# Kernel tuning notes

Measured on AMD Instinct MI355X. Metric: run time of the kernel, lower is better.

## Reference

```python
import jax, jax.numpy as jnp
import numpy as np

B, K, F_DIM, H_DIM, HEADS = 512, 17, 256, 256, 4
N = B * K           # 8704 flattened nodes
E = 139264          # edges (avg degree 16)
NEG_SLOPE = 0.2


def setup_inputs() -> dict:
    key = jax.random.key(0)
    ks = jax.random.split(key, 12)
    s_in = 1.0 / np.sqrt(F_DIM)
    s_hid = 1.0 / np.sqrt(H_DIM)
    return {
        "kpt_feature": jax.random.normal(ks[0], (B, K, F_DIM), jnp.float32),
        "edge_index": jax.random.randint(ks[1], (2, E), 0, N, jnp.int64),
        # conv1: F_DIM -> HEADS x H_DIM, concat=False (mean)
        "W1": jax.random.normal(ks[2], (F_DIM, HEADS * H_DIM), jnp.float32) * s_in,
        "a_src1": jax.random.normal(ks[3], (HEADS, H_DIM), jnp.float32) * s_hid,
        "a_dst1": jax.random.normal(ks[4], (HEADS, H_DIM), jnp.float32) * s_hid,
        "b1": jnp.zeros((H_DIM,), jnp.float32),
        # conv2: H_DIM -> HEADS x F_DIM, concat=False (mean)
        "W2": jax.random.normal(ks[5], (H_DIM, HEADS * F_DIM), jnp.float32) * s_hid,
        "a_src2": jax.random.normal(ks[6], (HEADS, F_DIM), jnp.float32) * s_in,
        "a_dst2": jax.random.normal(ks[7], (HEADS, F_DIM), jnp.float32) * s_in,
        "b2": jnp.zeros((F_DIM,), jnp.float32),
    }


def gat_conv(x, src, dst, W, a_src, a_dst, bias):
    # x: [N, Fin]; src/dst: [E'] (self-loops included); W: [Fin, H*C]
    n = x.shape[0]
    heads, c = a_src.shape
    h = (x @ W).reshape(n, heads, c)                       # [N,H,C]
    alpha_src = jnp.einsum("nhc,hc->nh", h, a_src)         # [N,H]
    alpha_dst = jnp.einsum("nhc,hc->nh", h, a_dst)
    e = jax.nn.leaky_relu(alpha_src[src] + alpha_dst[dst], NEG_SLOPE)  # [E',H]
    # segment softmax over incoming edges of each destination node
    emax = jax.ops.segment_max(e, dst, num_segments=n)
    emax = jnp.where(jnp.isfinite(emax), emax, 0.0)
    ex = jnp.exp(e - emax[dst])
    denom = jax.ops.segment_sum(ex, dst, num_segments=n)
    alpha = ex / denom[dst]                                # [E',H]
    msg = alpha[:, :, None] * h[src]                       # [E',H,C]
    out = jax.ops.segment_sum(msg, dst, num_segments=n)    # [N,H,C]
    return out.mean(axis=1) + bias                         # concat=False -> mean


def reference(kpt_feature, edge_index, W1, a_src1, a_dst1, b1, W2, a_src2, a_dst2, b2):
    b, k, f = kpt_feature.shape
    n = b * k
    x = kpt_feature.reshape(n, f)
    loop = jnp.arange(n, dtype=edge_index.dtype)
    src = jnp.concatenate([edge_index[0], loop])  # PyG add_self_loops=True
    dst = jnp.concatenate([edge_index[1], loop])
    x = gat_conv(x, src, dst, W1, a_src1, a_dst1, b1)
    x = jax.nn.relu(x)
    x = gat_conv(x, src, dst, W2, a_src2, a_dst2, b2)
    return x.reshape(b, k, f)
```

## Files before the change

kernel.cpp:

```cpp
#include <hip/hip_runtime.h>
#include <hip/hip_fp16.h>
#include <math.h>

#define NNODES 8704
#define NEDGE  139264
#define EPLUS  (NEDGE + NNODES)
#define NEG_SLOPE 0.2f
#define DEGCAP 64
#define LDSK   40

#define NB_PV  16
#define NB_WC  512
#define NB_SC  ((EPLUS + 255) / 256)
#define NB_AL  (NNODES / 4)

typedef _Float16 f16x8 __attribute__((ext_vector_type(8)));
typedef _Float16 f16x4 __attribute__((ext_vector_type(4)));
typedef float    f32x4 __attribute__((ext_vector_type(4)));

__device__ __forceinline__ float lrelu(float v) { return v >= 0.f ? v : NEG_SLOPE * v; }

__global__ __launch_bounds__(256) void prep_all(const float* __restrict__ W1,
                                                const float* __restrict__ as1,
                                                const float* __restrict__ ad1,
                                                const float* __restrict__ W2,
                                                const float* __restrict__ as2,
                                                const float* __restrict__ ad2,
                                                float* __restrict__ pbuf,
                                                int* __restrict__ cnt,
                                                float* __restrict__ alphasB,
                                                _Float16* __restrict__ Wc1,
                                                _Float16* __restrict__ Wc2) {
    __shared__ float tile[32][33];
    const int b = blockIdx.x;
    const int t = threadIdx.x;
    if (b < NB_PV) {
        for (int i = b * 256 + t; i < NNODES; i += NB_PV * 256) cnt[i] = 0;
        for (int i = b * 256 + t; i < NNODES * 8; i += NB_PV * 256) alphasB[i] = 0.f;
        float* a_sh = &tile[0][0];
        const int layer = b >> 3, sd = (b >> 2) & 1, h = b & 3;
        const float* W  = layer ? W2 : W1;
        const float* av = layer ? (sd ? ad2 : as2) : (sd ? ad1 : as1);
        a_sh[t] = av[h * 256 + t];
        __syncthreads();
        float acc = 0.f;
        const float* Wr = W + (size_t)t * 1024 + h * 256;
#pragma unroll 8
        for (int c = 0; c < 256; ++c) acc += Wr[c] * a_sh[c];
        pbuf[b * 256 + t] = acc;
    } else {
        const int idx = b - NB_PV;
        const int k0 = (idx & 7) * 32, o0 = ((idx >> 3) & 7) * 32;
        const int z = idx >> 6;
        const int layer = z >> 2, h = z & 3;
        const float* W = layer ? W2 : W1;
        _Float16* Wc   = layer ? Wc2 : Wc1;
#pragma unroll
        for (int p = 0; p < 4; ++p) {
            int e = t + p * 256; int kk = e >> 5, oo = e & 31;
            tile[kk][oo] = W[(size_t)(k0 + kk) * 1024 + h * 256 + o0 + oo];
        }
        __syncthreads();
#pragma unroll
        for (int p = 0; p < 4; ++p) {
            int e = t + p * 256; int oo = e >> 5, kk = e & 31;
            Wc[(size_t)(o0 + oo) * 1024 + h * 256 + k0 + kk] = (_Float16)tile[kk][oo];
        }
    }
}

__global__ __launch_bounds__(256) void scatter_alpha(const int* __restrict__ ei,
                                                     int* __restrict__ cnt,
                                                     int* __restrict__ csr,
                                                     const float* __restrict__ xf,
                                                     _Float16* __restrict__ xh_out,
                                                     const float* __restrict__ p ,
                                                     float* __restrict__ asrc,
                                                     float* __restrict__ adst) {
    const int b = blockIdx.x;
    const int t = threadIdx.x;
    if (b < NB_SC) {
        int e = b * 256 + t;
        if (e >= EPLUS) return;
        int src, dst;
        if (e < NEDGE) { src = ei[e]; dst = ei[NEDGE + e]; }
        else           { src = dst = e - NEDGE; }
        int slot = atomicAdd(&cnt[dst], 1);
        if (slot < DEGCAP) csr[dst * DEGCAP + slot] = src;
    } else {
        const int wave = t >> 6, l = t & 63;
        const int n = (b - NB_SC) * 4 + wave;
        float4 pv[8];
#pragma unroll
        for (int v = 0; v < 8; ++v) pv[v] = *(const float4*)(p + v * 256 + l * 4);
        float4 xv = *(const float4*)(xf + (size_t)n * 256 + l * 4);
        f16x4 hv = {(_Float16)xv.x, (_Float16)xv.y, (_Float16)xv.z, (_Float16)xv.w};
        *(f16x4*)(xh_out + (size_t)n * 256 + l * 4) = hv;
        float d[8];
#pragma unroll
        for (int v = 0; v < 8; ++v)
            d[v] = xv.x * pv[v].x + xv.y * pv[v].y + xv.z * pv[v].z + xv.w * pv[v].w;
#pragma unroll
        for (int off = 1; off <= 32; off <<= 1)
#pragma unroll
            for (int v = 0; v < 8; ++v) d[v] += __shfl_xor(d[v], off);
        if (l == 0) {
            *(float4*)(asrc + n * 4) = make_float4(d[0], d[1], d[2], d[3]);
            *(float4*)(adst + n * 4) = make_float4(d[4], d[5], d[6], d[7]);
        }
    }
}

__global__ __launch_bounds__(256) void agg_gather(const _Float16* __restrict__ xh,
                                                  const int* __restrict__ cnt,
                                                  const int* __restrict__ csr,
                                                  const float* __restrict__ asrc,
                                                  const float* __restrict__ adst,
                                                  _Float16* __restrict__ y) {
    const int w = threadIdx.x >> 6, l = threadIdx.x & 63;
    const int n = blockIdx.x * 4 + w;
    int deg = cnt[n]; if (deg > DEGCAP) deg = DEGCAP;

    float4 ad = *(const float4*)(adst + n * 4);
    int src_l = 0;
    float w0 = 0.f, w1 = 0.f, w2 = 0.f, w3 = 0.f;
    if (l < deg) {
        src_l = csr[n * DEGCAP + l];
        float4 as = *(const float4*)(asrc + src_l * 4);
        w0 = __expf(lrelu(as.x + ad.x));
        w1 = __expf(lrelu(as.y + ad.y));
        w2 = __expf(lrelu(as.z + ad.z));
        w3 = __expf(lrelu(as.w + ad.w));
    }
    float d0 = w0, d1 = w1, d2 = w2, d3 = w3;
#pragma unroll
    for (int off = 32; off >= 1; off >>= 1) {
        d0 += __shfl_xor(d0, off);
        d1 += __shfl_xor(d1, off);
        d2 += __shfl_xor(d2, off);
        d3 += __shfl_xor(d3, off);
    }
    w0 /= d0; w1 /= d1; w2 /= d2; w3 /= d3;

    const _Float16* xbase = xh + l * 4;
    float acc[4][4] = {};
    f16x4 xb[8], xn[8];
#pragma unroll
    for (int j = 0; j < 8; ++j) {
        int src = __shfl(src_l, j);
        if (j < deg) xb[j] = *(const f16x4*)(xbase + (size_t)src * 256);
    }
    for (int base = 0; base < deg; base += 8) {
#pragma unroll
        for (int j = 0; j < 8; ++j) {
            int s = base + 8 + j;
            int src = __shfl(src_l, s & 63);
            if (s < deg) xn[j] = *(const f16x4*)(xbase + (size_t)src * 256);
        }
#pragma unroll
        for (int j = 0; j < 8; ++j) {
            int s = base + j;
            if (s < deg) {
                float u0 = __shfl(w0, s), u1 = __shfl(w1, s);
                float u2 = __shfl(w2, s), u3 = __shfl(w3, s);
                f16x4 xv = xb[j];
#pragma unroll
                for (int c = 0; c < 4; ++c) {
                    float v = (float)xv[c];
                    acc[c][0] += u0 * v; acc[c][1] += u1 * v;
                    acc[c][2] += u2 * v; acc[c][3] += u3 * v;
                }
            }
        }
#pragma unroll
        for (int j = 0; j < 8; ++j) xb[j] = xn[j];
    }
#pragma unroll
    for (int h = 0; h < 4; ++h) {
        f16x4 pv = {(_Float16)acc[0][h], (_Float16)acc[1][h],
                    (_Float16)acc[2][h], (_Float16)acc[3][h]};
        *(f16x4*)(y + (size_t)n * 1024 + h * 256 + l * 4) = pv;
    }
}

__global__ __launch_bounds__(256) void gemm_out(const _Float16* __restrict__ Y,
                                                const _Float16* __restrict__ Wcatt,
                                                const float* __restrict__ bias,
                                                const float* __restrict__ p2,
                                                _Float16* __restrict__ outH,
                                                float* __restrict__ outF,
                                                float* __restrict__ asrc2,
                                                float* __restrict__ adst2) {
    __shared__ __align__(16) _Float16 As[2][64 * LDSK];
    __shared__ __align__(16) _Float16 Bs[2][128 * LDSK];
    __shared__ float p2s[8 * 128];
    const int t    = threadIdx.x;
    const int lane = t & 63;
    const int wave = t >> 6;
    const int wwr = wave >> 1, wwc = wave & 1;
    const int bm = blockIdx.x * 64;
    const int bn = blockIdx.y * 128;
    const int l15 = lane & 15, kb = lane >> 4;

    const int ar = t >> 2, ag = t & 3;
    const int br0 = t >> 2, br1 = 64 + (t >> 2), bg = t & 3;
    const _Float16* Yb  = Y     + (size_t)(bm + ar) * 1024 + ag * 8;
    const _Float16* Wb0 = Wcatt + (size_t)(bn + br0) * 1024 + bg * 8;
    const _Float16* Wb1 = Wcatt + (size_t)(bn + br1) * 1024 + bg * 8;
    const int aw = ar * LDSK + ag * 8;
    const int bw0 = br0 * LDSK + bg * 8, bw1 = br1 * LDSK + bg * 8;

    if (p2) {
#pragma unroll
        for (int p = 0; p < 4; ++p) {
            int e = t + p * 256;
            p2s[e] = p2[(e >> 7) * 256 + bn + (e & 127)];
        }
    }

    {
        f16x8 a0 = *(const f16x8*)(Yb);
        f16x8 b0 = *(const f16x8*)(Wb0);
        f16x8 b1 = *(const f16x8*)(Wb1);
        *(f16x8*)(&As[0][aw])  = a0;
        *(f16x8*)(&Bs[0][bw0]) = b0;
        *(f16x8*)(&Bs[0][bw1]) = b1;
    }
    f16x8 a_s0 = *(const f16x8*)(Yb + 32);
    f16x8 bb_s0[2] = { *(const f16x8*)(Wb0 + 32), *(const f16x8*)(Wb1 + 32) };
    f16x8 a_s1 = *(const f16x8*)(Yb + 64);
    f16x8 bb_s1[2] = { *(const f16x8*)(Wb0 + 64), *(const f16x8*)(Wb1 + 64) };
    __syncthreads();

    f32x4 acc[2][4] = {};
    int a_off[2], b_off[4];
#pragma unroll
    for (int i = 0; i < 2; ++i) a_off[i] = (wwr * 32 + i * 16 + l15) * LDSK + kb * 8;
#pragma unroll
    for (int j = 0; j < 4; ++j) b_off[j] = (wwc * 64 + j * 16 + l15) * LDSK + kb * 8;

    for (int h = 0; h < 32; h += 2) {
        {
            f16x8 af[2], bf[4];
#pragma unroll
            for (int i = 0; i < 2; ++i) af[i] = *(const f16x8*)(&As[0][a_off[i]]);
#pragma unroll
            for (int j = 0; j < 4; ++j) bf[j] = *(const f16x8*)(&Bs[0][b_off[j]]);
#pragma unroll
            for (int i = 0; i < 2; ++i)
#pragma unroll
                for (int j = 0; j < 4; ++j)
                    acc[i][j] = __builtin_amdgcn_mfma_f32_16x16x32_f16(af[i], bf[j], acc[i][j], 0, 0, 0);
            *(f16x8*)(&As[1][aw])  = a_s0;
            *(f16x8*)(&Bs[1][bw0]) = bb_s0[0];
            *(f16x8*)(&Bs[1][bw1]) = bb_s0[1];
            if (h + 3 < 32) {
                int k = (h + 3) * 32;
                a_s0 = *(const f16x8*)(Yb + k);
                bb_s0[0] = *(const f16x8*)(Wb0 + k);
                bb_s0[1] = *(const f16x8*)(Wb1 + k);
            }
            __syncthreads();
        }
        {
            f16x8 af[2], bf[4];
#pragma unroll
            for (int i = 0; i < 2; ++i) af[i] = *(const f16x8*)(&As[1][a_off[i]]);
#pragma unroll
            for (int j = 0; j < 4; ++j) bf[j] = *(const f16x8*)(&Bs[1][b_off[j]]);
#pragma unroll
            for (int i = 0; i < 2; ++i)
#pragma unroll
                for (int j = 0; j < 4; ++j)
                    acc[i][j] = __builtin_amdgcn_mfma_f32_16x16x32_f16(af[i], bf[j], acc[i][j], 0, 0, 0);
            if (h + 2 < 32) {
                *(f16x8*)(&As[0][aw])  = a_s1;
                *(f16x8*)(&Bs[0][bw0]) = bb_s1[0];
                *(f16x8*)(&Bs[0][bw1]) = bb_s1[1];
            }
            if (h + 4 < 32) {
                int k = (h + 4) * 32;
                a_s1 = *(const f16x8*)(Yb + k);
                bb_s1[0] = *(const f16x8*)(Wb0 + k);
                bb_s1[1] = *(const f16x8*)(Wb1 + k);
            }
            __syncthreads();
        }
    }

#pragma unroll
    for (int i = 0; i < 2; ++i)
#pragma unroll
        for (int q = 0; q < 4; ++q) {
            int row = bm + wwr * 32 + i * 16 + kb * 4 + q;
            float rv[4];
#pragma unroll
            for (int j = 0; j < 4; ++j) {
                int cl = wwc * 64 + j * 16 + l15;
                float r = 0.25f * acc[i][j][q] + bias[bn + cl];
                rv[j] = r;
                if (outH) outH[(size_t)row * 256 + bn + cl] = (_Float16)fmaxf(r, 0.f);
                else      outF[(size_t)row * 256 + bn + cl] = r;
            }
            if (p2) {
#pragma unroll
                for (int v = 0; v < 8; ++v) {
                    float ps = 0.f;
#pragma unroll
                    for (int j = 0; j < 4; ++j) {
                        int cl = wwc * 64 + j * 16 + l15;
                        ps += fmaxf(rv[j], 0.f) * p2s[v * 128 + cl];
                    }
#pragma unroll
                    for (int off = 1; off <= 8; off <<= 1) ps += __shfl_xor(ps, off);
                    if (l15 == 0) {
                        if (v < 4) atomicAdd(&asrc2[row * 4 + v], ps);
                        else       atomicAdd(&adst2[row * 4 + (v - 4)], ps);
                    }
                }
            }
        }
}

extern "C" void kernel_launch(void* const* d_in, const int* in_sizes, int n_in,
                              void* d_out, int out_size, void* d_ws, size_t ws_size,
                              hipStream_t stream) {
    const float* x0  = (const float*)d_in[0];
    const int*   ei  = (const int*)d_in[1];
    const float* W1  = (const float*)d_in[2];
    const float* as1 = (const float*)d_in[3];
    const float* ad1 = (const float*)d_in[4];
    const float* b1  = (const float*)d_in[5];
    const float* W2  = (const float*)d_in[6];
    const float* as2 = (const float*)d_in[7];
    const float* ad2 = (const float*)d_in[8];
    const float* b2  = (const float*)d_in[9];
    float* out = (float*)d_out;

    char* w = (char*)d_ws;
    _Float16* y   = (_Float16*)w; w += (size_t)NNODES * 1024 * 2;
    _Float16* x0h = (_Float16*)w; w += (size_t)NNODES * 256 * 2;
    _Float16* x1h = (_Float16*)w; w += (size_t)NNODES * 256 * 2;
    _Float16* Wc1 = (_Float16*)w; w += (size_t)256 * 1024 * 2;
    _Float16* Wc2 = (_Float16*)w; w += (size_t)256 * 1024 * 2;
    float* pbuf   = (float*)w;    w += 16 * 256 * 4;
    float* asrcA  = (float*)w;    w += NNODES * 4 * 4;
    float* adstA  = (float*)w;    w += NNODES * 4 * 4;
    float* alphasB = (float*)w;   w += NNODES * 8 * 4;
    float* asrcB  = alphasB;
    float* adstB  = alphasB + NNODES * 4;
    int* cnt      = (int*)w;      w += NNODES * 4;
    int* csr      = (int*)w;      w += (size_t)NNODES * DEGCAP * 4;

    const dim3 gemm_grid(NNODES / 64, 2);

    prep_all<<<NB_PV + NB_WC, 256, 0, stream>>>(W1, as1, ad1, W2, as2, ad2,
                                                pbuf, cnt, alphasB, Wc1, Wc2);
    scatter_alpha<<<NB_SC + NB_AL, 256, 0, stream>>>(ei, cnt, csr, x0, x0h, pbuf, asrcA, adstA);

    agg_gather<<<NNODES / 4, 256, 0, stream>>>(x0h, cnt, csr, asrcA, adstA, y);
    gemm_out<<<gemm_grid, 256, 0, stream>>>(y, Wc1, b1, pbuf + 8 * 256, x1h, nullptr, asrcB, adstB);

    agg_gather<<<NNODES / 4, 256, 0, stream>>>(x1h, cnt, csr, asrcB, adstB, y);
    gemm_out<<<gemm_grid, 256, 0, stream>>>(y, Wc2, b2, nullptr, nullptr, out, nullptr, nullptr);
}
```

Measured before the change: 123.8 us.

## Fuse all GAT stages into one cooperative persistent kernel with grid syncs

Replaces the six separate kernel launches with a single cooperative persistent kernel of 512 blocks that runs prep, CSR scatter/alpha, aggregation and GEMM phases in sequence, separated by grid-wide barriers. Work is distributed with grid-stride loops, and the GEMM phase uses only the first 272 blocks. The goal is to remove per-launch overhead and inter-kernel gaps. In exchange it adds grid sync costs, leaves blocks idle during the GEMM phases, and caps occupancy at 2 blocks per CU. A fallback multi-kernel path runs if the cooperative launch fails.

```diff
diff --git a/kernel.cpp b/kernel.cpp
--- a/kernel.cpp
+++ b/kernel.cpp
@@ -1,6 +1,9 @@
 #include <hip/hip_runtime.h>
 #include <hip/hip_fp16.h>
+#include <hip/hip_cooperative_groups.h>
 #include <math.h>
+
+namespace cg = cooperative_groups;
 
 #define NNODES 8704
 #define NEDGE  139264
@@ -8,11 +11,9 @@
 #define NEG_SLOPE 0.2f
 #define DEGCAP 64
 #define LDSK   40
-
-#define NB_PV  16
-#define NB_WC  512
-#define NB_SC  ((EPLUS + 255) / 256)
-#define NB_AL  (NNODES / 4)
+#define GRID   512
+#define BLK    256
+#define SMEM_BYTES 34816
 
 typedef _Float16 f16x8 __attribute__((ext_vector_type(8)));
 typedef _Float16 f16x4 __attribute__((ext_vector_type(4)));
@@ -20,82 +21,71 @@
 
 __device__ __forceinline__ float lrelu(float v) { return v >= 0.f ? v : NEG_SLOPE * v; }
 
-__global__ __launch_bounds__(256) void prep_all(const float* __restrict__ W1,
-                                                const float* __restrict__ as1,
-                                                const float* __restrict__ ad1,
-                                                const float* __restrict__ W2,
-                                                const float* __restrict__ as2,
-                                                const float* __restrict__ ad2,
-                                                float* __restrict__ pbuf,
-                                                int* __restrict__ cnt,
-                                                float* __restrict__ alphasB,
-                                                _Float16* __restrict__ Wc1,
-                                                _Float16* __restrict__ Wc2) {
-    __shared__ float tile[32][33];
-    const int b = blockIdx.x;
-    const int t = threadIdx.x;
-    if (b < NB_PV) {
-        for (int i = b * 256 + t; i < NNODES; i += NB_PV * 256) cnt[i] = 0;
-        for (int i = b * 256 + t; i < NNODES * 8; i += NB_PV * 256) alphasB[i] = 0.f;
-        float* a_sh = &tile[0][0];
-        const int layer = b >> 3, sd = (b >> 2) & 1, h = b & 3;
-        const float* W  = layer ? W2 : W1;
-        const float* av = layer ? (sd ? ad2 : as2) : (sd ? ad1 : as1);
-        a_sh[t] = av[h * 256 + t];
+
+__device__ __forceinline__ void phase_prep(int b, int t,
+        const float* W1, const float* as1, const float* ad1,
+        const float* W2, const float* as2, const float* ad2,
+        float* pbuf, int* cnt, float* alphasB,
+        _Float16* Wc1, _Float16* Wc2, char* smem) {
+    if (b < 16) {
+        for (int i = b * 256 + t; i < NNODES; i += 16 * 256) cnt[i] = 0;
+        for (int i = b * 256 + t; i < NNODES * 8; i += 16 * 256) alphasB[i] = 0.f;
+    }
+    for (int u = b; u < 528; u += GRID) {
         __syncthreads();
-        float acc = 0.f;
-        const float* Wr = W + (size_t)t * 1024 + h * 256;
+        if (u < 16) {
+            float* a_sh = (float*)smem;
+            const int layer = u >> 3, sd = (u >> 2) & 1, h = u & 3;
+            const float* W  = layer ? W2 : W1;
+            const float* av = layer ? (sd ? ad2 : as2) : (sd ? ad1 : as1);
+            a_sh[t] = av[h * 256 + t];
+            __syncthreads();
+            float acc = 0.f;
+            const float* Wr = W + (size_t)t * 1024 + h * 256;
 #pragma unroll 8
-        for (int c = 0; c < 256; ++c) acc += Wr[c] * a_sh[c];
-        pbuf[b * 256 + t] = acc;
-    } else {
-        const int idx = b - NB_PV;
-        const int k0 = (idx & 7) * 32, o0 = ((idx >> 3) & 7) * 32;
-        const int z = idx >> 6;
-        const int layer = z >> 2, h = z & 3;
-        const float* W = layer ? W2 : W1;
-        _Float16* Wc   = layer ? Wc2 : Wc1;
-#pragma unroll
-        for (int p = 0; p < 4; ++p) {
-            int e = t + p * 256; int kk = e >> 5, oo = e & 31;
-            tile[kk][oo] = W[(size_t)(k0 + kk) * 1024 + h * 256 + o0 + oo];
-        }
-        __syncthreads();
-#pragma unroll
-        for (int p = 0; p < 4; ++p) {
-            int e = t + p * 256; int oo = e >> 5, kk = e & 31;
-            Wc[(size_t)(o0 + oo) * 1024 + h * 256 + k0 + kk] = (_Float16)tile[kk][oo];
-        }
-    }
-}
-
-__global__ __launch_bounds__(256) void scatter_alpha(const int* __restrict__ ei,
-                                                     int* __restrict__ cnt,
-                                                     int* __restrict__ csr,
-                                                     const float* __restrict__ xf,
-                                                     _Float16* __restrict__ xh_out,
-                                                     const float* __restrict__ p ,
-                                                     float* __restrict__ asrc,
-                                                     float* __restrict__ adst) {
-    const int b = blockIdx.x;
-    const int t = threadIdx.x;
-    if (b < NB_SC) {
-        int e = b * 256 + t;
-        if (e >= EPLUS) return;
+            for (int c = 0; c < 256; ++c) acc += Wr[c] * a_sh[c];
+            pbuf[u * 256 + t] = acc;
+        } else {
+            float (*tile)[33] = (float(*)[33])smem;
+            const int idx = u - 16;
+            const int k0 = (idx & 7) * 32, o0 = ((idx >> 3) & 7) * 32;
+            const int z = idx >> 6, layer = z >> 2, h = z & 3;
+            const float* W = layer ? W2 : W1;
+            _Float16* Wc   = layer ? Wc2 : Wc1;
+#pragma unroll
+            for (int p = 0; p < 4; ++p) {
+                int e = t + p * 256; int kk = e >> 5, oo = e & 31;
+                tile[kk][oo] = W[(size_t)(k0 + kk) * 1024 + h * 256 + o0 + oo];
+            }
+            __syncthreads();
+#pragma unroll
+            for (int p = 0; p < 4; ++p) {
+                int e = t + p * 256; int oo = e >> 5, kk = e & 31;
+                Wc[(size_t)(o0 + oo) * 1024 + h * 256 + k0 + kk] = (_Float16)tile[kk][oo];
+            }
+        }
+    }
+}
+
+__device__ __forceinline__ void phase_scatter_alpha(int b, int t,
+        const int* ei, int* cnt, int* csr,
+        const float* x0, _Float16* x0h, const float* pbuf,
+        float* asrc, float* adst) {
+    for (int e = b * BLK + t; e < EPLUS; e += GRID * BLK) {
         int src, dst;
         if (e < NEDGE) { src = ei[e]; dst = ei[NEDGE + e]; }
         else           { src = dst = e - NEDGE; }
         int slot = atomicAdd(&cnt[dst], 1);
         if (slot < DEGCAP) csr[dst * DEGCAP + slot] = src;
-    } else {
-        const int wave = t >> 6, l = t & 63;
-        const int n = (b - NB_SC) * 4 + wave;
-        float4 pv[8];
-#pragma unroll
-        for (int v = 0; v < 8; ++v) pv[v] = *(const float4*)(p + v * 256 + l * 4);
-        float4 xv = *(const float4*)(xf + (size_t)n * 256 + l * 4);
+    }
+    const int w = t >> 6, l = t & 63;
+    float4 pv[8];
+#pragma unroll
+    for (int v = 0; v < 8; ++v) pv[v] = *(const float4*)(pbuf + v * 256 + l * 4);
+    for (int n = b * 4 + w; n < NNODES; n += GRID * 4) {
+        float4 xv = *(const float4*)(x0 + (size_t)n * 256 + l * 4);
         f16x4 hv = {(_Float16)xv.x, (_Float16)xv.y, (_Float16)xv.z, (_Float16)xv.w};
-        *(f16x4*)(xh_out + (size_t)n * 256 + l * 4) = hv;
+        *(f16x4*)(x0h + (size_t)n * 256 + l * 4) = hv;
         float d[8];
 #pragma unroll
         for (int v = 0; v < 8; ++v)
@@ -111,95 +101,86 @@
     }
 }
 
-__global__ __launch_bounds__(256) void agg_gather(const _Float16* __restrict__ xh,
-                                                  const int* __restrict__ cnt,
-                                                  const int* __restrict__ csr,
-                                                  const float* __restrict__ asrc,
-                                                  const float* __restrict__ adst,
-                                                  _Float16* __restrict__ y) {
-    const int w = threadIdx.x >> 6, l = threadIdx.x & 63;
-    const int n = blockIdx.x * 4 + w;
-    int deg = cnt[n]; if (deg > DEGCAP) deg = DEGCAP;
-
-    float4 ad = *(const float4*)(adst + n * 4);
-    int src_l = 0;
-    float w0 = 0.f, w1 = 0.f, w2 = 0.f, w3 = 0.f;
-    if (l < deg) {
-        src_l = csr[n * DEGCAP + l];
-        float4 as = *(const float4*)(asrc + src_l * 4);
-        w0 = __expf(lrelu(as.x + ad.x));
-        w1 = __expf(lrelu(as.y + ad.y));
-        w2 = __expf(lrelu(as.z + ad.z));
-        w3 = __expf(lrelu(as.w + ad.w));
-    }
-    float d0 = w0, d1 = w1, d2 = w2, d3 = w3;
-#pragma unroll
-    for (int off = 32; off >= 1; off >>= 1) {
-        d0 += __shfl_xor(d0, off);
-        d1 += __shfl_xor(d1, off);
-        d2 += __shfl_xor(d2, off);
-        d3 += __shfl_xor(d3, off);
-    }
-    w0 /= d0; w1 /= d1; w2 /= d2; w3 /= d3;
-
+__device__ __forceinline__ void phase_agg(int b, int t,
+        const _Float16* xh, const int* cnt, const int* csr,
+        const float* asrc, const float* adst, _Float16* y) {
+    const int w = t >> 6, l = t & 63;
     const _Float16* xbase = xh + l * 4;
-    float acc[4][4] = {};
-    f16x4 xb[8], xn[8];
-#pragma unroll
-    for (int j = 0; j < 8; ++j) {
-        int src = __shfl(src_l, j);
-        if (j < deg) xb[j] = *(const f16x4*)(xbase + (size_t)src * 256);
-    }
-    for (int base = 0; base < deg; base += 8) {
+    for (int n = b * 4 + w; n < NNODES; n += GRID * 4) {
+        int deg = cnt[n]; if (deg > DEGCAP) deg = DEGCAP;
+        float4 ad = *(const float4*)(adst + n * 4);
+        int src_l = 0;
+        float w0 = 0.f, w1 = 0.f, w2 = 0.f, w3 = 0.f;
+        if (l < deg) {
+            src_l = csr[n * DEGCAP + l];
+            float4 as = *(const float4*)(asrc + src_l * 4);
+            w0 = __expf(lrelu(as.x + ad.x));
+            w1 = __expf(lrelu(as.y + ad.y));
+            w2 = __expf(lrelu(as.z + ad.z));
+            w3 = __expf(lrelu(as.w + ad.w));
+        }
+        float d0 = w0, d1 = w1, d2 = w2, d3 = w3;
+#pragma unroll
+        for (int off = 32; off >= 1; off >>= 1) {
+            d0 += __shfl_xor(d0, off);
+            d1 += __shfl_xor(d1, off);
+            d2 += __shfl_xor(d2, off);
+            d3 += __shfl_xor(d3, off);
+        }
+        w0 /= d0; w1 /= d1; w2 /= d2; w3 /= d3;
+
+        float acc[4][4] = {};
+        f16x4 xb[8], xn[8];
 #pragma unroll
         for (int j = 0; j < 8; ++j) {
-            int s = base + 8 + j;
-            int src = __shfl(src_l, s & 63);
-            if (s < deg) xn[j] = *(const f16x4*)(xbase + (size_t)src * 256);
-        }
-#pragma unroll
-        for (int j = 0; j < 8; ++j) {
-            int s = base + j;
-            if (s < deg) {
-                float u0 = __shfl(w0, s), u1 = __shfl(w1, s);
-                float u2 = __shfl(w2, s), u3 = __shfl(w3, s);
-                f16x4 xv = xb[j];
-#pragma unroll
-                for (int c = 0; c < 4; ++c) {
-                    float v = (float)xv[c];
-                    acc[c][0] += u0 * v; acc[c][1] += u1 * v;
-                    acc[c][2] += u2 * v; acc[c][3] += u3 * v;
+            int src = __shfl(src_l, j);
+            if (j < deg) xb[j] = *(const f16x4*)(xbase + (size_t)src * 256);
+        }
+        for (int base = 0; base < deg; base += 8) {
+#pragma unroll
+            for (int j = 0; j < 8; ++j) {
+                int s = base + 8 + j;
+                int src = __shfl(src_l, s & 63);
+                if (s < deg) xn[j] = *(const f16x4*)(xbase + (size_t)src * 256);
+            }
+#pragma unroll
+            for (int j = 0; j < 8; ++j) {
+                int s = base + j;
+                if (s < deg) {
+                    float u0 = __shfl(w0, s), u1 = __shfl(w1, s);
+                    float u2 = __shfl(w2, s), u3 = __shfl(w3, s);
+                    f16x4 xv = xb[j];
+#pragma unroll
+                    for (int c = 0; c < 4; ++c) {
+                        float v = (float)xv[c];
+                        acc[c][0] += u0 * v; acc[c][1] += u1 * v;
+                        acc[c][2] += u2 * v; acc[c][3] += u3 * v;
+                    }
                 }
             }
-        }
-#pragma unroll
-        for (int j = 0; j < 8; ++j) xb[j] = xn[j];
-    }
-#pragma unroll
-    for (int h = 0; h < 4; ++h) {
-        f16x4 pv = {(_Float16)acc[0][h], (_Float16)acc[1][h],
-                    (_Float16)acc[2][h], (_Float16)acc[3][h]};
-        *(f16x4*)(y + (size_t)n * 1024 + h * 256 + l * 4) = pv;
-    }
-}
-
-__global__ __launch_bounds__(256) void gemm_out(const _Float16* __restrict__ Y,
-                                                const _Float16* __restrict__ Wcatt,
-                                                const float* __restrict__ bias,
-                                                const float* __restrict__ p2,
-                                                _Float16* __restrict__ outH,
-                                                float* __restrict__ outF,
-                                                float* __restrict__ asrc2,
-                                                float* __restrict__ adst2) {
-    __shared__ __align__(16) _Float16 As[2][64 * LDSK];
-    __shared__ __align__(16) _Float16 Bs[2][128 * LDSK];
-    __shared__ float p2s[8 * 128];
-    const int t    = threadIdx.x;
+#pragma unroll
+            for (int j = 0; j < 8; ++j) xb[j] = xn[j];
+        }
+#pragma unroll
+        for (int h = 0; h < 4; ++h) {
+            f16x4 pv = {(_Float16)acc[0][h], (_Float16)acc[1][h],
+                        (_Float16)acc[2][h], (_Float16)acc[3][h]};
+            *(f16x4*)(y + (size_t)n * 1024 + h * 256 + l * 4) = pv;
+        }
+    }
+}
+
+__device__ __forceinline__ void gemm_tile(const _Float16* __restrict__ Y,
+        const _Float16* __restrict__ Wcatt, const float* __restrict__ bias,
+        const float* __restrict__ p2, _Float16* __restrict__ outH,
+        float* __restrict__ outF, float* __restrict__ asrc2, float* __restrict__ adst2,
+        int bm, int bn, int t, char* smem) {
+    _Float16* As = (_Float16*)smem;
+    _Float16* Bs = (_Float16*)(smem + 10240);
+    float* p2s   = (float*)(smem + 30720);
     const int lane = t & 63;
     const int wave = t >> 6;
     const int wwr = wave >> 1, wwc = wave & 1;
-    const int bm = blockIdx.x * 64;
-    const int bn = blockIdx.y * 128;
     const int l15 = lane & 15, kb = lane >> 4;
 
     const int ar = t >> 2, ag = t & 3;
@@ -222,9 +203,9 @@
         f16x8 a0 = *(const f16x8*)(Yb);
         f16x8 b0 = *(const f16x8*)(Wb0);
         f16x8 b1 = *(const f16x8*)(Wb1);
-        *(f16x8*)(&As[0][aw])  = a0;
-        *(f16x8*)(&Bs[0][bw0]) = b0;
-        *(f16x8*)(&Bs[0][bw1]) = b1;
+        *(f16x8*)(&As[aw])  = a0;
+        *(f16x8*)(&Bs[bw0]) = b0;
+        *(f16x8*)(&Bs[bw1]) = b1;
     }
     f16x8 a_s0 = *(const f16x8*)(Yb + 32);
     f16x8 bb_s0[2] = { *(const f16x8*)(Wb0 + 32), *(const f16x8*)(Wb1 + 32) };
@@ -243,17 +224,17 @@
         {
             f16x8 af[2], bf[4];
 #pragma unroll
-            for (int i = 0; i < 2; ++i) af[i] = *(const f16x8*)(&As[0][a_off[i]]);
-#pragma unroll
-            for (int j = 0; j < 4; ++j) bf[j] = *(const f16x8*)(&Bs[0][b_off[j]]);
+            for (int i = 0; i < 2; ++i) af[i] = *(const f16x8*)(&As[a_off[i]]);
+#pragma unroll
+            for (int j = 0; j < 4; ++j) bf[j] = *(const f16x8*)(&Bs[b_off[j]]);
 #pragma unroll
             for (int i = 0; i < 2; ++i)
 #pragma unroll
                 for (int j = 0; j < 4; ++j)
                     acc[i][j] = __builtin_amdgcn_mfma_f32_16x16x32_f16(af[i], bf[j], acc[i][j], 0, 0, 0);
-            *(f16x8*)(&As[1][aw])  = a_s0;
-            *(f16x8*)(&Bs[1][bw0]) = bb_s0[0];
-            *(f16x8*)(&Bs[1][bw1]) = bb_s0[1];
+            *(f16x8*)(&As[2560 + aw])  = a_s0;
+            *(f16x8*)(&Bs[5120 + bw0]) = bb_s0[0];
+            *(f16x8*)(&Bs[5120 + bw1]) = bb_s0[1];
             if (h + 3 < 32) {
                 int k = (h + 3) * 32;
                 a_s0 = *(const f16x8*)(Yb + k);
@@ -265,18 +246,18 @@
         {
             f16x8 af[2], bf[4];
 #pragma unroll
-            for (int i = 0; i < 2; ++i) af[i] = *(const f16x8*)(&As[1][a_off[i]]);
-#pragma unroll
-            for (int j = 0; j < 4; ++j) bf[j] = *(const f16x8*)(&Bs[1][b_off[j]]);
+            for (int i = 0; i < 2; ++i) af[i] = *(const f16x8*)(&As[2560 + a_off[i]]);
+#pragma unroll
+            for (int j = 0; j < 4; ++j) bf[j] = *(const f16x8*)(&Bs[5120 + b_off[j]]);
 #pragma unroll
             for (int i = 0; i < 2; ++i)
 #pragma unroll
                 for (int j = 0; j < 4; ++j)
                     acc[i][j] = __builtin_amdgcn_mfma_f32_16x16x32_f16(af[i], bf[j], acc[i][j], 0, 0, 0);
             if (h + 2 < 32) {
-                *(f16x8*)(&As[0][aw])  = a_s1;
-                *(f16x8*)(&Bs[0][bw0]) = bb_s1[0];
-                *(f16x8*)(&Bs[0][bw1]) = bb_s1[1];
+                *(f16x8*)(&As[aw])  = a_s1;
+                *(f16x8*)(&Bs[bw0]) = bb_s1[0];
+                *(f16x8*)(&Bs[bw1]) = bb_s1[1];
             }
             if (h + 4 < 32) {
                 int k = (h + 4) * 32;
@@ -320,6 +301,55 @@
                 }
             }
         }
+}
+
+__global__ __launch_bounds__(BLK, 2) void mega(const float* x0, const int* ei,
+        const float* W1, const float* as1, const float* ad1, const float* b1,
+        const float* W2, const float* as2, const float* ad2, const float* b2,
+        float* out, _Float16* y, _Float16* x0h, _Float16* x1h,
+        _Float16* Wc1, _Float16* Wc2, float* pbuf,
+        float* asrcA, float* adstA, float* asrcB, float* adstB,
+        int* cnt, int* csr) {
+    cg::grid_group grid = cg::this_grid();
+    __shared__ __align__(16) char smem[SMEM_BYTES];
+    const int b = blockIdx.x, t = threadIdx.x;
+
+    phase_prep(b, t, W1, as1, ad1, W2, as2, ad2, pbuf, cnt, asrcB, Wc1, Wc2, smem);
+    grid.sync();
+    phase_scatter_alpha(b, t, ei, cnt, csr, x0, x0h, pbuf, asrcA, adstA);
+    grid.sync();
+    phase_agg(b, t, x0h, cnt, csr, asrcA, adstA, y);
+    grid.sync();
+    if (b < 272) gemm_tile(y, Wc1, b1, pbuf + 2048, x1h, nullptr, asrcB, adstB,
+                           (b >> 1) * 64, (b & 1) * 128, t, smem);
+    grid.sync();
+    phase_agg(b, t, x1h, cnt, csr, asrcB, adstB, y);
+    grid.sync();
+    if (b < 272) gemm_tile(y, Wc2, b2, nullptr, nullptr, out, nullptr, nullptr,
+                           (b >> 1) * 64, (b & 1) * 128, t, smem);
+}
+
+__global__ __launch_bounds__(BLK) void k_prep(const float* W1, const float* as1, const float* ad1,
+        const float* W2, const float* as2, const float* ad2,
+        float* pbuf, int* cnt, float* alphasB, _Float16* Wc1, _Float16* Wc2) {
+    __shared__ __align__(16) char smem[SMEM_BYTES];
+    phase_prep(blockIdx.x, threadIdx.x, W1, as1, ad1, W2, as2, ad2, pbuf, cnt, alphasB, Wc1, Wc2, smem);
+}
+__global__ __launch_bounds__(BLK) void k_scatter_alpha(const int* ei, int* cnt, int* csr,
+        const float* x0, _Float16* x0h, const float* pbuf, float* asrc, float* adst) {
+    phase_scatter_alpha(blockIdx.x, threadIdx.x, ei, cnt, csr, x0, x0h, pbuf, asrc, adst);
+}
+__global__ __launch_bounds__(BLK) void k_agg(const _Float16* xh, const int* cnt, const int* csr,
+        const float* asrc, const float* adst, _Float16* y) {
+    phase_agg(blockIdx.x, threadIdx.x, xh, cnt, csr, asrc, adst, y);
+}
+__global__ __launch_bounds__(BLK) void k_gemm(const _Float16* Y, const _Float16* Wcatt,
+        const float* bias, const float* p2, _Float16* outH, float* outF,
+        float* asrc2, float* adst2) {
+    __shared__ __align__(16) char smem[SMEM_BYTES];
+    if (blockIdx.x < 272)
+        gemm_tile(Y, Wcatt, bias, p2, outH, outF, asrc2, adst2,
+                  ((int)blockIdx.x >> 1) * 64, ((int)blockIdx.x & 1) * 128, threadIdx.x, smem);
 }
 
 extern "C" void kernel_launch(void* const* d_in, const int* in_sizes, int n_in,
@@ -352,15 +382,21 @@
     int* cnt      = (int*)w;      w += NNODES * 4;
     int* csr      = (int*)w;      w += (size_t)NNODES * DEGCAP * 4;
 
-    const dim3 gemm_grid(NNODES / 64, 2);
-
-    prep_all<<<NB_PV + NB_WC, 256, 0, stream>>>(W1, as1, ad1, W2, as2, ad2,
-                                                pbuf, cnt, alphasB, Wc1, Wc2);
-    scatter_alpha<<<NB_SC + NB_AL, 256, 0, stream>>>(ei, cnt, csr, x0, x0h, pbuf, asrcA, adstA);
-
-    agg_gather<<<NNODES / 4, 256, 0, stream>>>(x0h, cnt, csr, asrcA, adstA, y);
-    gemm_out<<<gemm_grid, 256, 0, stream>>>(y, Wc1, b1, pbuf + 8 * 256, x1h, nullptr, asrcB, adstB);
-
-    agg_gather<<<NNODES / 4, 256, 0, stream>>>(x1h, cnt, csr, asrcB, adstB, y);
-    gemm_out<<<gemm_grid, 256, 0, stream>>>(y, Wc2, b2, nullptr, nullptr, out, nullptr, nullptr);
-}
+    void* args[] = { (void*)&x0, (void*)&ei, (void*)&W1, (void*)&as1, (void*)&ad1, (void*)&b1,
+                     (void*)&W2, (void*)&as2, (void*)&ad2, (void*)&b2,
+                     (void*)&out, (void*)&y, (void*)&x0h, (void*)&x1h,
+                     (void*)&Wc1, (void*)&Wc2, (void*)&pbuf,
+                     (void*)&asrcA, (void*)&adstA, (void*)&asrcB, (void*)&adstB,
+                     (void*)&cnt, (void*)&csr };
+    hipError_t err = hipLaunchCooperativeKernel((const void*)mega, dim3(GRID), dim3(BLK),
+                                                args, 0, stream);
+    if (err != hipSuccess) {
+        (void)hipGetLastError();
+        k_prep<<<GRID, BLK, 0, stream>>>(W1, as1, ad1, W2, as2, ad2, pbuf, cnt, alphasB, Wc1, Wc2);
+        k_scatter_alpha<<<GRID, BLK, 0, stream>>>(ei, cnt, csr, x0, x0h, pbuf, asrcA, adstA);
+        k_agg<<<GRID, BLK, 0, stream>>>(x0h, cnt, csr, asrcA, adstA, y);
+        k_gemm<<<272, BLK, 0, stream>>>(y, Wc1, b1, pbuf + 2048, x1h, nullptr, asrcB, adstB);
+        k_agg<<<GRID, BLK, 0, stream>>>(x1h, cnt, csr, asrcB, adstB, y);
+        k_gemm<<<272, BLK, 0, stream>>>(y, Wc2, b2, nullptr, nullptr, out, nullptr, nullptr);
+    }
+}
```

Result: slower. 428.7 us (+246.3%).
